# Performance work log

Measured on AMD Instinct MI355X. Metric: run time of the kernel, lower is better.

## Reference

```python
import jax, jax.numpy as jnp
import numpy as np

HIDDEN = 4096
N_HEADS = 32
N_KV_HEADS = 8
D_HEAD = HIDDEN // N_HEADS  # 128
SEQ_LEN = 2048
ROPE_THETA = 10000.0


def _rope(t, start_index):
    # t: [L, n_heads, d_head]; rotate-half (Llama-style) RoPE
    L, _, d = t.shape
    inv_freq = 1.0 / (ROPE_THETA ** (jnp.arange(0, d, 2, dtype=jnp.float32) / d))  # [d/2]
    pos = jnp.arange(L, dtype=jnp.float32) + jnp.float32(start_index)  # [L]
    ang = pos[:, None] * inv_freq  # [L, d/2]
    cos = jnp.cos(ang)[:, None, :].astype(t.dtype)  # [L, 1, d/2]
    sin = jnp.sin(ang)[:, None, :].astype(t.dtype)
    t1, t2 = jnp.split(t, 2, axis=-1)
    return jnp.concatenate([t1 * cos - t2 * sin, t1 * sin + t2 * cos], axis=-1)


def setup_inputs() -> dict:
    key = jax.random.key(0)
    ks = jax.random.split(key, 5)
    s = 1.0 / np.sqrt(HIDDEN)
    return {
        "x": jax.random.normal(ks[0], (SEQ_LEN, HIDDEN), dtype=jnp.float32),
        "Wq": jax.random.normal(ks[1], (HIDDEN, N_HEADS * D_HEAD), dtype=jnp.float32) * s,
        "Wk": jax.random.normal(ks[2], (HIDDEN, N_KV_HEADS * D_HEAD), dtype=jnp.float32) * s,
        "Wv": jax.random.normal(ks[3], (HIDDEN, N_KV_HEADS * D_HEAD), dtype=jnp.float32) * s,
        "Wo": jax.random.normal(ks[4], (N_HEADS * D_HEAD, HIDDEN), dtype=jnp.float32) * s,
        "start_index": 0,
    }


def reference(x, Wq, Wk, Wv, Wo, start_index):
    # x: [L, hidden]; start_index==0 -> cache reset, so post-write cache == current k, v
    L, _ = x.shape
    q = (x @ Wq).reshape(L, N_HEADS, D_HEAD)
    k = (x @ Wk).reshape(L, N_KV_HEADS, D_HEAD)
    v = (x @ Wv).reshape(L, N_KV_HEADS, D_HEAD)
    q = _rope(q, start_index)
    k = _rope(k, start_index)
    # KV cache read: full cache is just [L] entries (prefill)
    S = L
    g = N_HEADS // N_KV_HEADS
    qh = q.transpose(1, 0, 2).reshape(N_KV_HEADS, g, L, D_HEAD)  # [kv, g, L, d]
    kh = k.transpose(1, 0, 2)  # [kv, S, d]
    vh = v.transpose(1, 0, 2)  # [kv, S, d]
    scale = 1.0 / np.sqrt(D_HEAD)
    scores = jnp.einsum('kgld,ksd->kgls', qh, kh) * jnp.asarray(scale, qh.dtype)
    # is_causal = (L > 1): tril(L, S) mask
    causal = jnp.tril(jnp.ones((L, S), dtype=bool))
    neg = jnp.asarray(jnp.finfo(scores.dtype).min, scores.dtype)
    scores = jnp.where(causal, scores, neg)
    attn = jax.nn.softmax(scores, axis=-1)
    out = jnp.einsum('kgls,ksd->kgld', attn, vh)  # [kv, g, L, d]
    out = out.reshape(N_HEADS, L, D_HEAD).transpose(1, 0, 2).reshape(L, N_HEADS * D_HEAD)
    return out @ Wo
```

## Files before the change

kernel.cpp:

```cpp
#include <hip/hip_runtime.h>

typedef unsigned short u16;
typedef float f32x4 __attribute__((ext_vector_type(4)));
typedef __bf16 bf16x8 __attribute__((ext_vector_type(8)));
typedef u16 u16x8 __attribute__((ext_vector_type(8)));

static __device__ __forceinline__ u16 f2bf(float f) {
  union { float f; unsigned u; } v; v.f = f;
  unsigned r = v.u + 0x7fffu + ((v.u >> 16) & 1u);
  return (u16)(r >> 16);
}
static __device__ __forceinline__ float bf2f(u16 x) {
  union { unsigned u; float f; } v; v.u = (unsigned)x << 16; return v.f;
}

static __device__ __forceinline__ f32x4 mfma16(u16x8 a, u16x8 b, f32x4 c) {
  return __builtin_amdgcn_mfma_f32_16x16x32_bf16(
      __builtin_bit_cast(bf16x8, a), __builtin_bit_cast(bf16x8, b), c, 0, 0, 0);
}

static __device__ __forceinline__ void load_lds16(const void* g, void* l) {
  __builtin_amdgcn_global_load_lds(
      (const __attribute__((address_space(1))) void*)g,
      (__attribute__((address_space(3))) void*)l, 16, 0, 0);
}

__global__ void cvt_f32_bf16_swz(const float* __restrict__ in, u16* __restrict__ out, int n8) {
  int i = blockIdx.x * blockDim.x + threadIdx.x;
  if (i >= n8) return;
  int row = i >> 9;
  int j = i & 511;
  int jp = (j & ~7) | ((j & 7) ^ (row & 7));
  const float* src = in + (size_t)i * 8;
  u16x8 o;
  #pragma unroll
  for (int e = 0; e < 8; e++) o[e] = f2bf(src[e]);
  *(u16x8*)(out + ((size_t)row << 12) + jp * 8) = o;
}

__global__ __launch_bounds__(256)
void transpose_cvt(const float* __restrict__ W, u16* __restrict__ Wt, int K, int N) {
  __shared__ float tile[32][33];
  int tx = threadIdx.x & 31, ty = threadIdx.x >> 5;
  int k0 = blockIdx.x * 32, n0 = blockIdx.y * 32;
  #pragma unroll
  for (int i = ty; i < 32; i += 8)
    tile[i][tx] = W[(size_t)(k0 + i) * N + (n0 + tx)];
  __syncthreads();
  #pragma unroll
  for (int i = ty; i < 32; i += 8) {
    int n = n0 + i;
    int k = k0 + tx;
    Wt[(size_t)n * K + (k ^ ((n & 7) * 8))] = f2bf(tile[tx][i]);
  }
}

__global__ void rope_table_k(float2* __restrict__ tab, const int* __restrict__ start, int L) {
  int i = blockIdx.x * blockDim.x + threadIdx.x;
  if (i >= L * 64) return;
  int p = i >> 6, j = i & 63;
  float inv = powf(10000.0f, -(float)j / 64.0f);
  float ang = (float)(p + start[0]) * inv;
  tab[i] = make_float2(cosf(ang), sinf(ang));
}

__global__ void rope_apply_b(const u16* __restrict__ in, int istride, int icol,
                             u16* __restrict__ outp, const float2* __restrict__ tab,
                             int total, int H, float scale, int swz) {
  int i = blockIdx.x * blockDim.x + threadIdx.x;
  if (i >= total) return;
  int j8 = (i & 7) * 8;
  int h = (i >> 3) % H;
  int p = i / (8 * H);
  const u16* base = in + (size_t)p * istride + icol + h * 128;
  u16x8 a = *(const u16x8*)(base + j8);
  u16x8 b = *(const u16x8*)(base + j8 + 64);
  u16x8 o1, o2;
  #pragma unroll
  for (int e = 0; e < 8; e++) {
    float2 cs = tab[p * 64 + j8 + e];
    float av = bf2f(a[e]), bv = bf2f(b[e]);
    o1[e] = f2bf((av * cs.x - bv * cs.y) * scale);
    o2[e] = f2bf((av * cs.y + bv * cs.x) * scale);
  }
  int c1 = i & 7;
  int cs1 = swz ? (c1 ^ (p & 7)) : c1;
  u16* ob = outp + ((size_t)p * H + h) * 128 + cs1 * 8;
  *(u16x8*)ob = o1;
  *(u16x8*)(ob + 64) = o2;
}

template<int BN, bool OUT_BF16>
__global__ __launch_bounds__(512, 2)
void gemm8p(const u16* __restrict__ A, const u16* __restrict__ Bt,
            float* __restrict__ Cf, u16* __restrict__ Cb, int N, int K, int gm) {
  constexpr int N_REP = BN / 64;
  constexpr int NHALF = N_REP / 2;
  constexpr int STR = 16 * NHALF;
  constexpr int BJP = (BN == 256) ? 2 : 1;
  __shared__ alignas(16) u16 As[2][256 * 64];
  __shared__ alignas(16) u16 Bs[2][BN * 64];
  const int tid = threadIdx.x;
  const int lane = tid & 63;
  const int wid = tid >> 6;
  const int ql = lane & 15, kg = lane >> 4;
  const int wr = wid >> 2, wcn = wid & 3;

  const int nb = gridDim.x;
  const int b = blockIdx.x;
  const int swz = (b & 7) * (nb >> 3) + (b >> 3);
  const int m0 = (swz % gm) * 256;
  const int n0 = (swz / gm) * BN;

  const int srow = tid >> 3, schk = tid & 7;
  const u16* abase = A + (size_t)(m0 + srow) * K + schk * 8;
  const u16* bbase = Bt + (size_t)n0 * K + schk * 8;

  auto stageA = [&](int buf, int t, int qa) {
    load_lds16(abase + (size_t)(qa * 64) * K + t * 64,
               &As[buf][((qa * 64 + srow) * 8 + schk) * 8]);
  };
  auto stageB = [&](int buf, int t, int n2, int jp) {
    int j = jp * (64 / STR) + srow / STR;
    int r = srow % STR;
    int g = j * (2 * STR) + n2 * STR + r;
    load_lds16(bbase + (size_t)g * K + t * 64,
               &Bs[buf][((n2 * (BN / 2) + jp * 64 + srow) * 8 + schk) * 8]);
  };

  f32x4 acc[8][N_REP] = {};
  u16x8 af[4][2];
  u16x8 bfr[2][NHALF][2];
  const int NT = K / 64;

  stageA(0, 0, 0); stageA(0, 0, 2);
  #pragma unroll
  for (int jp = 0; jp < BJP; jp++) stageB(0, 0, 0, jp);
  #pragma unroll
  for (int jp = 0; jp < BJP; jp++) stageB(0, 0, 1, jp);
  stageA(0, 0, 1); stageA(0, 0, 3);
  asm volatile("s_waitcnt vmcnt(0)" ::: "memory");
  __builtin_amdgcn_sched_barrier(0);
  __builtin_amdgcn_s_barrier();

  #pragma unroll 1
  for (int i = 0; i < NT / 2; i++) {
    #pragma unroll
    for (int p = 0; p < 8; p++) {
      const int q = p & 3;
      const int m = q >> 1, n2 = q & 1;
      const int cbuf = (p < 4) ? 0 : 1;
      if constexpr (BN == 256)
        asm volatile("s_waitcnt vmcnt(4)" ::: "memory");
      else
        asm volatile("s_waitcnt vmcnt(2)" ::: "memory");
      __builtin_amdgcn_sched_barrier(0);
      if (q == 0 || q == 2) {
        #pragma unroll
        for (int mi = 0; mi < 4; mi++)
          #pragma unroll
          for (int kk = 0; kk < 2; kk++) {
            int row = wr * 128 + m * 64 + mi * 16 + ql;
            int ch = ((kk << 2) | kg) ^ (ql & 7);
            af[mi][kk] = *(const u16x8*)&As[cbuf][(row * 8 + ch) * 8];
          }
      }
      if (q == 0 || q == 1) {
        #pragma unroll
        for (int ni = 0; ni < NHALF; ni++)
          #pragma unroll
          for (int kk = 0; kk < 2; kk++) {
            int R = q * (BN / 2) + wcn * STR + ni * 16 + ql;
            int ch = ((kk << 2) | kg) ^ (ql & 7);
            bfr[q][ni][kk] = *(const u16x8*)&Bs[cbuf][(R * 8 + ch) * 8];
          }
      }
      const int st = 2 * i + 1 + (p >= 4 ? 1 : 0);
      const int sbuf = st & 1;
      if (st < NT) {
        if (q == 0) { stageA(sbuf, st, 0); stageA(sbuf, st, 2); }
        else if (q == 1) {
          #pragma unroll
          for (int jp = 0; jp < BJP; jp++) stageB(sbuf, st, 0, jp);
        } else if (q == 2) {
          #pragma unroll
          for (int jp = 0; jp < BJP; jp++) stageB(sbuf, st, 1, jp);
        } else { stageA(sbuf, st, 1); stageA(sbuf, st, 3); }
      }
      __builtin_amdgcn_sched_barrier(0);
      __builtin_amdgcn_s_barrier();
      __builtin_amdgcn_sched_barrier(0);
      __builtin_amdgcn_s_setprio(1);
      #pragma unroll
      for (int mi = 0; mi < 4; mi++)
        #pragma unroll
        for (int ni = 0; ni < NHALF; ni++)
          #pragma unroll
          for (int kk = 0; kk < 2; kk++)
            acc[m * 4 + mi][n2 * NHALF + ni] =
                mfma16(af[mi][kk], bfr[n2][ni][kk], acc[m * 4 + mi][n2 * NHALF + ni]);
      __builtin_amdgcn_s_setprio(0);
      __builtin_amdgcn_sched_barrier(0);
      __builtin_amdgcn_s_barrier();
    }
  }
  asm volatile("s_waitcnt vmcnt(0)" ::: "memory");

  #pragma unroll
  for (int mi = 0; mi < 8; mi++) {
    #pragma unroll
    for (int ni = 0; ni < N_REP; ni++) {
      int row0 = m0 + wr * 128 + mi * 16 + kg * 4;
      int col = n0 + wcn * (16 * N_REP) + ni * 16 + ql;
      #pragma unroll
      for (int r = 0; r < 4; r++) {
        if constexpr (OUT_BF16)
          Cb[(size_t)(row0 + r) * N + col] = f2bf(acc[mi][ni][r]);
        else
          Cf[(size_t)(row0 + r) * N + col] = acc[mi][ni][r];
      }
    }
  }
}

__global__ __launch_bounds__(256, 2)
void attn_k(const u16* __restrict__ qr, const u16* __restrict__ kr,
            const u16* __restrict__ qkv, u16* __restrict__ out) {
  __shared__ alignas(16) u16 Kls[2][64 * 128];
  __shared__ alignas(16) u16 Vt[2][128][72];
  __shared__ alignas(16) u16 Plds[4][16][72];
  const int tid = threadIdx.x;
  const int lane = tid & 63, wave = tid >> 6;
  const int ql = lane & 15, kg = lane >> 4;
  const int h = blockIdx.y, hk = h >> 2;

  const int sl4 = (tid & 15) * 4;
  const int d0s = (tid >> 4) * 8;
  const u16* vbase = qkv + 5120 + (size_t)hk * 128 + d0s;
  const int krow_s = tid >> 4, kcol_s = (tid & 15) * 8;
  const u16* kbase = kr + (size_t)hk * 128 + (size_t)krow_s * 1024 + kcol_s;

  int cur = 0;
  #pragma unroll 1
  for (int half_idx = 0; half_idx < 2; half_idx++) {
    const int tile = half_idx ? (31 - (int)blockIdx.x) : (int)blockIdx.x;
    const int q0 = tile * 64;
    const int qw = q0 + wave * 16;
    const int nsteps = tile + 1;

    u16x8 qf[4];
    const u16* qbase = qr + ((size_t)(qw + ql) * 32 + h) * 128;
    #pragma unroll
    for (int kk = 0; kk < 4; kk++)
      qf[kk] = *(const u16x8*)(qbase + kk * 32 + kg * 8);

    f32x4 acc[8] = {};
    float m_run = -3e38f, l_run = 0.f;

    __syncthreads();
    cur = 0;
    #pragma unroll
    for (int r = 0; r < 4; r++)
      load_lds16(kbase + (size_t)r * 16 * 1024, &Kls[0][(r * 256 + tid) * 8]);
    u16x8 vreg[4];
    #pragma unroll
    for (int j = 0; j < 4; j++)
      vreg[j] = *(const u16x8*)(vbase + (size_t)(sl4 + j) * 6144);

    #pragma unroll 1
    for (int t = 0; t < nsteps; t++) {
      const int s0 = t * 64;
      #pragma unroll
      for (int e = 0; e < 8; e++) {
        ushort4 w;
        w.x = vreg[0][e]; w.y = vreg[1][e]; w.z = vreg[2][e]; w.w = vreg[3][e];
        *(ushort4*)&Vt[cur][d0s + e][sl4] = w;
      }
      __syncthreads();
      if (t + 1 < nsteps) {
        const u16* kn = kbase + (size_t)(s0 + 64) * 1024;
        #pragma unroll
        for (int r = 0; r < 4; r++)
          load_lds16(kn + (size_t)r * 16 * 1024, &Kls[cur ^ 1][(r * 256 + tid) * 8]);
        #pragma unroll
        for (int j = 0; j < 4; j++)
          vreg[j] = *(const u16x8*)(vbase + (size_t)(s0 + 64 + sl4 + j) * 6144);
      }
      f32x4 sc[4] = {};
      __builtin_amdgcn_s_setprio(1);
      #pragma unroll
      for (int sb = 0; sb < 4; sb++) {
        const u16* krow = &Kls[cur][(sb * 16 + ql) * 128];
        #pragma unroll
        for (int kk = 0; kk < 4; kk++) {
          u16x8 kf = *(const u16x8*)(krow + (((kk * 4 + kg) ^ (ql & 7)) * 8));
          sc[sb] = mfma16(kf, qf[kk], sc[sb]);
        }
      }
      __builtin_amdgcn_s_setprio(0);
      const int qg = qw + ql;
      float mt = -3e38f;
      #pragma unroll
      for (int sb = 0; sb < 4; sb++)
        #pragma unroll
        for (int r = 0; r < 4; r++) {
          int s = s0 + sb * 16 + kg * 4 + r;
          float v = (s > qg) ? -3e38f : sc[sb][r];
          sc[sb][r] = v;
          mt = fmaxf(mt, v);
        }
      mt = fmaxf(mt, __shfl_xor(mt, 16, 64));
      mt = fmaxf(mt, __shfl_xor(mt, 32, 64));
      if (!__all(mt - m_run <= 11.5f)) {
        float m_new = fmaxf(m_run, mt);
        float fco = exp2f(m_run - m_new);
        float fr[4];
        #pragma unroll
        for (int r = 0; r < 4; r++) fr[r] = __shfl(fco, (lane & 48) | (kg * 4 + r), 64);
        #pragma unroll
        for (int db = 0; db < 8; db++)
          #pragma unroll
          for (int r = 0; r < 4; r++) acc[db][r] *= fr[r];
        l_run *= fco;
        m_run = m_new;
      }
      float rs = 0.f;
      #pragma unroll
      for (int sb = 0; sb < 4; sb++)
        #pragma unroll
        for (int r = 0; r < 4; r++) {
          float e = exp2f(sc[sb][r] - m_run);
          sc[sb][r] = e;
          rs += e;
        }
      rs += __shfl_xor(rs, 16, 64);
      rs += __shfl_xor(rs, 32, 64);
      l_run += rs;
      #pragma unroll
      for (int sb = 0; sb < 4; sb++) {
        ushort4 pk;
        pk.x = f2bf(sc[sb][0]); pk.y = f2bf(sc[sb][1]);
        pk.z = f2bf(sc[sb][2]); pk.w = f2bf(sc[sb][3]);
        *(ushort4*)&Plds[wave][ql][sb * 16 + kg * 4] = pk;
      }
      __builtin_amdgcn_s_setprio(1);
      #pragma unroll
      for (int hf = 0; hf < 2; hf++) {
        u16x8 pf = *(const u16x8*)&Plds[wave][ql][hf * 32 + kg * 8];
        #pragma unroll
        for (int db = 0; db < 8; db++) {
          u16x8 vf = *(const u16x8*)&Vt[cur][db * 16 + ql][hf * 32 + kg * 8];
          acc[db] = mfma16(pf, vf, acc[db]);
        }
      }
      __builtin_amdgcn_s_setprio(0);
      cur ^= 1;
    }

    float linv[4];
    #pragma unroll
    for (int r = 0; r < 4; r++)
      linv[r] = 1.f / __shfl(l_run, (lane & 48) | (kg * 4 + r), 64);
    #pragma unroll
    for (int db = 0; db < 8; db++) {
      int d = db * 16 + ql;
      #pragma unroll
      for (int r = 0; r < 4; r++) {
        int q = qw + kg * 4 + r;
        int col = (h * 128 + d) ^ ((q & 7) << 3);
        out[(size_t)q * 4096 + col] = f2bf(acc[db][r] * linv[r]);
      }
    }
  }
}

extern "C" void kernel_launch(void* const* d_in, const int* in_sizes, int n_in,
                              void* d_out, int out_size, void* d_ws, size_t ws_size,
                              hipStream_t stream) {
  const float* x  = (const float*)d_in[0];
  const float* Wq = (const float*)d_in[1];
  const float* Wk = (const float*)d_in[2];
  const float* Wv = (const float*)d_in[3];
  const float* Wo = (const float*)d_in[4];
  const int* start = (const int*)d_in[5];

  const int L = 2048, HID = 4096, NH = 32, NKV = 8;
  const int NQ = 4096, NKVD = 1024, NF = 6144;

  char* ws = (char*)d_ws;
  size_t off = 0;
  auto alloc = [&](size_t bytes) {
    void* p = ws + off;
    off += (bytes + 255) & ~(size_t)255;
    return p;
  };
  u16* x_b   = (u16*)alloc((size_t)L * HID * 2);
  u16* Wq_t  = (u16*)alloc((size_t)NQ * HID * 2);
  u16* Wk_t  = (u16*)alloc((size_t)NKVD * HID * 2);
  u16* Wv_t  = (u16*)alloc((size_t)NKVD * HID * 2);
  u16* Wo_t  = (u16*)alloc((size_t)HID * NQ * 2);
  u16* q_r   = (u16*)alloc((size_t)L * NQ * 2);
  u16* k_r   = (u16*)alloc((size_t)L * NKVD * 2);
  float2* tab = (float2*)alloc((size_t)L * 64 * sizeof(float2));
  u16* qkv_b  = (u16*)d_out;
  u16* attn_b = Wq_t;

  const float qscale = 0.08838834764831845f * 1.4426950408889634f;

  cvt_f32_bf16_swz<<<(L * HID / 8 + 255) / 256, 256, 0, stream>>>(x, x_b, L * HID / 8);
  transpose_cvt<<<dim3(HID / 32, NQ / 32), 256, 0, stream>>>(Wq, Wq_t, HID, NQ);
  transpose_cvt<<<dim3(HID / 32, NKVD / 32), 256, 0, stream>>>(Wk, Wk_t, HID, NKVD);
  transpose_cvt<<<dim3(HID / 32, NKVD / 32), 256, 0, stream>>>(Wv, Wv_t, HID, NKVD);
  transpose_cvt<<<dim3(NQ / 32, HID / 32), 256, 0, stream>>>(Wo, Wo_t, NQ, HID);
  rope_table_k<<<(L * 64 + 255) / 256, 256, 0, stream>>>(tab, start, L);

  gemm8p<256, true><<<192, 512, 0, stream>>>(x_b, Wq_t, nullptr, qkv_b, NF, HID, 8);

  rope_apply_b<<<(L * NH * 8 + 255) / 256, 256, 0, stream>>>(qkv_b, NF, 0, q_r, tab, L * NH * 8, NH, qscale, 0);
  rope_apply_b<<<(L * NKV * 8 + 255) / 256, 256, 0, stream>>>(qkv_b, NF, NQ, k_r, tab, L * NKV * 8, NKV, 1.0f, 1);

  attn_k<<<dim3(16, NH), 256, 0, stream>>>(q_r, k_r, qkv_b, attn_b);

  gemm8p<128, false><<<256, 512, 0, stream>>>(attn_b, Wo_t, (float*)d_out, nullptr, HID, NQ, 8);
}
```

Baseline: 376.2 us.

## Vectorize weight transpose-convert and refine GEMM vmcnt wait placement

The weight transpose kernel now reads float4 rows into a 128x32 tile and writes 16-byte swizzled bf16 chunks instead of scalar 2-byte stores, aiming to cut memory transactions in the per-call weight conversion. The GEMM's per-phase global-load wait moves after the next stage's loads are issued, uses per-phase counts, and adds an explicit tail drain plus an lgkmcnt wait after the barrier. The goal is more overlap of global-to-LDS loads with MFMA work. Wrong wait counts would risk reading stale LDS data.

```diff
diff --git a/kernel.cpp b/kernel.cpp
--- a/kernel.cpp
+++ b/kernel.cpp
@@ -4,6 +4,8 @@
 typedef float f32x4 __attribute__((ext_vector_type(4)));
 typedef __bf16 bf16x8 __attribute__((ext_vector_type(8)));
 typedef u16 u16x8 __attribute__((ext_vector_type(8)));
+
+#define VMCNT(n) asm volatile("s_waitcnt vmcnt(" #n ")" ::: "memory")
 
 static __device__ __forceinline__ u16 f2bf(float f) {
   union { float f; unsigned u; } v; v.f = f;
@@ -40,18 +42,28 @@
 
 __global__ __launch_bounds__(256)
 void transpose_cvt(const float* __restrict__ W, u16* __restrict__ Wt, int K, int N) {
-  __shared__ float tile[32][33];
-  int tx = threadIdx.x & 31, ty = threadIdx.x >> 5;
-  int k0 = blockIdx.x * 32, n0 = blockIdx.y * 32;
-  #pragma unroll
-  for (int i = ty; i < 32; i += 8)
-    tile[i][tx] = W[(size_t)(k0 + i) * N + (n0 + tx)];
+  __shared__ float tile[128][33];
+  const int k0 = blockIdx.x * 128, n0 = blockIdx.y * 32;
+  const int tr = threadIdx.x >> 3;
+  const int tc4 = (threadIdx.x & 7) * 4;
+  #pragma unroll
+  for (int it = 0; it < 4; it++) {
+    int kl = it * 32 + tr;
+    float4 v = *(const float4*)&W[(size_t)(k0 + kl) * N + n0 + tc4];
+    tile[kl][tc4] = v.x; tile[kl][tc4 + 1] = v.y;
+    tile[kl][tc4 + 2] = v.z; tile[kl][tc4 + 3] = v.w;
+  }
   __syncthreads();
-  #pragma unroll
-  for (int i = ty; i < 32; i += 8) {
-    int n = n0 + i;
-    int k = k0 + tx;
-    Wt[(size_t)n * K + (k ^ ((n & 7) * 8))] = f2bf(tile[tx][i]);
+  const int nl = threadIdx.x >> 4;
+  const int dch = threadIdx.x & 15;
+  #pragma unroll
+  for (int it = 0; it < 2; it++) {
+    int n = n0 + it * 16 + nl;
+    int sch = (dch & 8) | ((dch & 7) ^ (n & 7));
+    u16x8 o;
+    #pragma unroll
+    for (int e = 0; e < 8; e++) o[e] = f2bf(tile[sch * 8 + e][it * 16 + nl]);
+    *(u16x8*)&Wt[(size_t)n * K + k0 + dch * 8] = o;
   }
 }
 
@@ -95,7 +107,7 @@
 void gemm8p(const u16* __restrict__ A, const u16* __restrict__ Bt,
             float* __restrict__ Cf, u16* __restrict__ Cb, int N, int K, int gm) {
   constexpr int N_REP = BN / 64;
-  constexpr int NHALF = N_REP / 2;
+  constexpr int NHALF = N_REP / 2 > 0 ? N_REP / 2 : 1;
   constexpr int STR = 16 * NHALF;
   constexpr int BJP = (BN == 256) ? 2 : 1;
   __shared__ alignas(16) u16 As[2][256 * 64];
@@ -139,22 +151,18 @@
   #pragma unroll
   for (int jp = 0; jp < BJP; jp++) stageB(0, 0, 1, jp);
   stageA(0, 0, 1); stageA(0, 0, 3);
-  asm volatile("s_waitcnt vmcnt(0)" ::: "memory");
+  if constexpr (BN == 256) VMCNT(4); else VMCNT(3);
   __builtin_amdgcn_sched_barrier(0);
   __builtin_amdgcn_s_barrier();
 
   #pragma unroll 1
   for (int i = 0; i < NT / 2; i++) {
+    const bool tail = (i == NT / 2 - 1);
     #pragma unroll
     for (int p = 0; p < 8; p++) {
       const int q = p & 3;
       const int m = q >> 1, n2 = q & 1;
       const int cbuf = (p < 4) ? 0 : 1;
-      if constexpr (BN == 256)
-        asm volatile("s_waitcnt vmcnt(4)" ::: "memory");
-      else
-        asm volatile("s_waitcnt vmcnt(2)" ::: "memory");
-      __builtin_amdgcn_sched_barrier(0);
       if (q == 0 || q == 2) {
         #pragma unroll
         for (int mi = 0; mi < 4; mi++)
@@ -187,8 +195,22 @@
           for (int jp = 0; jp < BJP; jp++) stageB(sbuf, st, 1, jp);
         } else { stageA(sbuf, st, 1); stageA(sbuf, st, 3); }
       }
+      if (!tail || p < 4) {
+        if constexpr (BN == 256) {
+          VMCNT(4);
+        } else {
+          if (q == 0) VMCNT(4);
+          else if (q == 1) VMCNT(3);
+          else if (q == 2) VMCNT(2);
+          else VMCNT(3);
+        }
+      } else {
+        if (p == 4) VMCNT(2);
+        else if (p == 5) VMCNT(0);
+      }
       __builtin_amdgcn_sched_barrier(0);
       __builtin_amdgcn_s_barrier();
+      asm volatile("s_waitcnt lgkmcnt(0)" ::: "memory");
       __builtin_amdgcn_sched_barrier(0);
       __builtin_amdgcn_s_setprio(1);
       #pragma unroll
@@ -204,7 +226,6 @@
       __builtin_amdgcn_s_barrier();
     }
   }
-  asm volatile("s_waitcnt vmcnt(0)" ::: "memory");
 
   #pragma unroll
   for (int mi = 0; mi < 8; mi++) {
@@ -408,10 +429,10 @@
   const float qscale = 0.08838834764831845f * 1.4426950408889634f;
 
   cvt_f32_bf16_swz<<<(L * HID / 8 + 255) / 256, 256, 0, stream>>>(x, x_b, L * HID / 8);
-  transpose_cvt<<<dim3(HID / 32, NQ / 32), 256, 0, stream>>>(Wq, Wq_t, HID, NQ);
-  transpose_cvt<<<dim3(HID / 32, NKVD / 32), 256, 0, stream>>>(Wk, Wk_t, HID, NKVD);
-  transpose_cvt<<<dim3(HID / 32, NKVD / 32), 256, 0, stream>>>(Wv, Wv_t, HID, NKVD);
-  transpose_cvt<<<dim3(NQ / 32, HID / 32), 256, 0, stream>>>(Wo, Wo_t, NQ, HID);
+  transpose_cvt<<<dim3(HID / 128, NQ / 32), 256, 0, stream>>>(Wq, Wq_t, HID, NQ);
+  transpose_cvt<<<dim3(HID / 128, NKVD / 32), 256, 0, stream>>>(Wk, Wk_t, HID, NKVD);
+  transpose_cvt<<<dim3(HID / 128, NKVD / 32), 256, 0, stream>>>(Wv, Wv_t, HID, NKVD);
+  transpose_cvt<<<dim3(NQ / 128, HID / 32), 256, 0, stream>>>(Wo, Wo_t, NQ, HID);
   rope_table_k<<<(L * 64 + 255) / 256, 256, 0, stream>>>(tab, start, L);
 
   gemm8p<256, true><<<192, 512, 0, stream>>>(x_b, Wq_t, nullptr, qkv_b, NF, HID, 8);
```

New measurement: 362.6 us. -3.6%, faster.
